# Kernel tuning notes

Measured on AMD Instinct MI355X. Metric: run time of the kernel, lower is better.

The kernel has to match this reference:

```python
import jax, jax.numpy as jnp
import numpy as np

B, T, H = 16, 512, 384   # batch, phoneme length, hidden
F, K = 384, 3            # filter size, kernel size
DMAX = 8                 # max per-token duration
L = T * DMAX             # static max expanded length (original uses real_len.max())


def conv1d_same(x, w, b):
    # x: [B, T, Cin], w: [Cout, Cin, K] (torch OIW layout), padding = K//2 both sides
    y = jax.lax.conv_general_dilated(
        x.transpose(0, 2, 1), w, window_strides=(1,),
        padding=[(K // 2, K // 2)], dimension_numbers=('NCW', 'OIW', 'NCW'))
    return y.transpose(0, 2, 1) + b


def layer_norm(x, g, b, eps=1e-5):
    mu = jnp.mean(x, axis=-1, keepdims=True)
    var = jnp.mean(jnp.square(x - mu), axis=-1, keepdims=True)
    return (x - mu) * jax.lax.rsqrt(var + eps) * g + b


def setup_inputs() -> dict:
    key = jax.random.key(0)
    ks = jax.random.split(key, 10)
    x = jax.random.normal(ks[0], (B, T, H), dtype=jnp.float32)
    # log-durations whose exp().round() gives integers in [1, DMAX]
    dur = jax.random.randint(ks[1], (B, T), 1, DMAX + 1)
    true_durations = jnp.log(dur.astype(jnp.float32))
    s1 = 1.0 / np.sqrt(H * K)
    s2 = 1.0 / np.sqrt(F * K)
    s3 = 1.0 / np.sqrt(F)
    return {
        'x': x,
        'true_durations': true_durations,
        'conv1_w': jax.random.uniform(ks[2], (F, H, K), jnp.float32, -s1, s1),
        'conv1_b': jnp.zeros((F,), jnp.float32),
        'ln1_g': jnp.ones((F,), jnp.float32),
        'ln1_b': jnp.zeros((F,), jnp.float32),
        'conv2_w': jax.random.uniform(ks[3], (F, F, K), jnp.float32, -s2, s2),
        'conv2_b': jnp.zeros((F,), jnp.float32),
        'ln2_g': jnp.ones((F,), jnp.float32),
        'ln2_b': jnp.zeros((F,), jnp.float32),
        'lin_w': jax.random.uniform(ks[4], (F, 1), jnp.float32, -s3, s3),
        'lin_b': jnp.zeros((1,), jnp.float32),
    }


def reference(x, true_durations, conv1_w, conv1_b, ln1_g, ln1_b,
              conv2_w, conv2_b, ln2_g, ln2_b, lin_w, lin_b):
    # duration predictor net (dropout in eval mode = identity)
    h = conv1d_same(x, conv1_w, conv1_b)
    h = jax.nn.gelu(layer_norm(h, ln1_g, ln1_b), approximate=False)
    h = conv1d_same(h, conv2_w, conv2_b)
    h = jax.nn.gelu(layer_norm(h, ln2_g, ln2_b), approximate=False)
    length = jax.nn.relu(h @ lin_w + lin_b)[..., 0]  # [B, T]

    # length regulation with ground-truth durations (detached ints in original)
    dur = jnp.round(jnp.exp(true_durations)).astype(jnp.int32)  # [B, T]
    ends = jnp.cumsum(dur, axis=1)          # [B, T]
    starts = ends - dur                     # [B, T]
    k = jnp.arange(L)                       # [L]
    # binary alignment: A[b,t,l] = 1 iff starts[b,t] <= l < ends[b,t]
    A = ((k >= starts[..., None]) & (k < ends[..., None])).astype(x.dtype)  # [B,T,L]
    out = jnp.einsum('bth,btl->blh', x, A)  # = (x^T @ A)^T, [B, L, H]
    return out, length
```

## Files before the change

kernel.cpp:

```cpp
#include <hip/hip_runtime.h>
#include <stdint.h>

typedef unsigned short u16;
typedef unsigned int   u32;

#define B_    16
#define T_    512
#define H_    384
#define F_    384
#define DMAX_ 8
#define L_    4096
#define KD    1152
#define M_    8192

typedef __bf16 bf16x8 __attribute__((ext_vector_type(8)));
typedef float  f32x4  __attribute__((ext_vector_type(4)));

typedef __attribute__((address_space(1))) u32 gu32;
typedef __attribute__((address_space(3))) u32 lu32;

__device__ __forceinline__ void dma16(const void* g, void* l) {
    __builtin_amdgcn_global_load_lds((gu32*)(uintptr_t)g, (lu32*)(u32)(uintptr_t)l, 16, 0, 0);
}

__device__ __forceinline__ u16 f2b(float f) {
    union { float f; u32 i; } v; v.f = f;
    u32 x = v.i;
    return (u16)((x + 0x7fffu + ((x >> 16) & 1u)) >> 16);
}

__global__ void k_prep(const float* __restrict__ td, const float* __restrict__ w1,
                       const float* __restrict__ w2, const float* __restrict__ x,
                       int* __restrict__ tmap, u16* __restrict__ Wp1,
                       u16* __restrict__ Wp2, u16* __restrict__ xb,
                       u16* __restrict__ zp) {
    int blk = blockIdx.x, tid = threadIdx.x;
    if (blk < 16) {
        __shared__ int s[T_];
        int b = blk, t = tid;
        int d = (int)roundf(expf(td[b * T_ + t]));
        if (d < 0) d = 0; if (d > DMAX_) d = DMAX_;
        int v = d;
        s[t] = v;
        __syncthreads();
        for (int off = 1; off < T_; off <<= 1) {
            int add = (t >= off) ? s[t - off] : 0;
            __syncthreads();
            v += add;
            s[t] = v;
            __syncthreads();
        }
        int end = v, start = end - d;
        for (int i = start; i < end; ++i) tmap[b * L_ + i] = t;
        int total = s[T_ - 1];
        for (int l = total + t; l < L_; l += T_) tmap[b * L_ + l] = -1;
    } else if (blk == 16) {
        zp[tid] = 0;
    } else if (blk < 17 + 1728) {
        int j = (blk - 17) * 512 + tid;
        const int n = F_ * H_ * 3;
        const float* src = (j < n) ? w1 : w2;
        u16* dst         = (j < n) ? Wp1 : Wp2;
        int jj = (j < n) ? j : j - n;
        int f = jj / (H_ * 3);
        int rem = jj % (H_ * 3);
        int c = rem / 3, kk = rem % 3;
        dst[f * KD + kk * H_ + c] = f2b(src[jj]);
    } else {
        int v = (blk - 1745) * 512 + tid;
        float4 f = *(const float4*)(x + (size_t)v * 4);
        u16 o[4] = { f2b(f.x), f2b(f.y), f2b(f.z), f2b(f.w) };
        *(uint2*)(xb + (size_t)v * 4) = *(uint2*)o;
    }
}

#define CHT 3584
#define DBO 28672

__device__ __forceinline__ void gemm_core64(u16* smem, const u16* __restrict__ src,
                                            const u16* __restrict__ Wp,
                                            const u16* __restrict__ zp,
                                            int m0, int tid, f32x4 acc[2][6]) {
    int w = tid >> 6, lane = tid & 63;
    int quad = lane >> 4, l16 = lane & 15;
    int wm = w & 1, wn = w >> 1;

    int rowA = tid >> 3;
    int qlA  = (tid & 7) ^ (rowA & 7);
    int arow = m0 + rowA;
    int bB = arow >> 9, tt = arow & 511;
    const u16* abase[3];
    #pragma unroll
    for (int kk = 0; kk < 3; ++kk) {
        int ts = tt + kk - 1;
        abase[kk] = (ts >= 0 && ts < T_) ? (src + (size_t)((bB << 9) + ts) * H_ + qlA * 8)
                                         : (zp + qlA * 8);
    }
    int adst = tid * 8;
    const u16* bbase[6];
    int bdst[6];
    #pragma unroll
    for (int p = 0; p < 6; ++p) {
        int idx = p * 512 + tid;
        int rowB = idx >> 3;
        int qlB  = (tid & 7) ^ (rowB & 7);
        bbase[p] = Wp + (size_t)rowB * KD + qlB * 8;
        bdst[p]  = (512 + idx) * 8;
    }

    int aoff[2][2], boff[6][2];
    #pragma unroll
    for (int i = 0; i < 2; ++i)
        #pragma unroll
        for (int kv = 0; kv < 2; ++kv) {
            int row = wm * 32 + i * 16 + l16;
            aoff[i][kv] = ((row << 3) | ((kv * 4 + quad) ^ (row & 7))) * 8;
        }
    #pragma unroll
    for (int j = 0; j < 6; ++j)
        #pragma unroll
        for (int kv = 0; kv < 2; ++kv) {
            int row = wn * 96 + j * 16 + l16;
            boff[j][kv] = (512 + ((row << 3) | ((kv * 4 + quad) ^ (row & 7)))) * 8;
        }

    #pragma unroll
    for (int i = 0; i < 2; ++i)
        #pragma unroll
        for (int j = 0; j < 6; ++j)
            acc[i][j] = f32x4{0.f, 0.f, 0.f, 0.f};

    {
        u16* base = smem;
        #pragma unroll
        for (int p = 0; p < 6; ++p) dma16(bbase[p], base + bdst[p]);
        dma16(abase[0], base + adst);
    }

    int kk1 = 0, s61 = 0;
    for (int s = 0; s < 18; ++s) {
        __syncthreads();
        if (s < 17) {
            if (++s61 == 6) { s61 = 0; ++kk1; }
            int koff = (s + 1) * 64;
            u16* base = smem + (((s + 1) & 1) ? DBO : 0);
            #pragma unroll
            for (int p = 0; p < 6; ++p) dma16(bbase[p] + koff, base + bdst[p]);
            dma16(abase[kk1] + s61 * 64, base + adst);
        }
        const u16* rb = smem + ((s & 1) ? DBO : 0);
        #pragma unroll
        for (int kv = 0; kv < 2; ++kv) {
            bf16x8 af0 = *(const bf16x8*)(rb + aoff[0][kv]);
            bf16x8 af1 = *(const bf16x8*)(rb + aoff[1][kv]);
            #pragma unroll
            for (int j = 0; j < 6; ++j) {
                bf16x8 bf = *(const bf16x8*)(rb + boff[j][kv]);
                acc[0][j] = __builtin_amdgcn_mfma_f32_16x16x32_bf16(af0, bf, acc[0][j], 0, 0, 0);
                acc[1][j] = __builtin_amdgcn_mfma_f32_16x16x32_bf16(af1, bf, acc[1][j], 0, 0, 0);
            }
        }
    }
    __syncthreads();
}

__launch_bounds__(512)
__global__ void k_main1(const u16* __restrict__ xb, const u16* __restrict__ Wp,
                        const float* __restrict__ bias, const float* __restrict__ g,
                        const float* __restrict__ beta, u16* __restrict__ G,
                        const u16* __restrict__ zp, const float* __restrict__ x,
                        const int* __restrict__ tmap, float* __restrict__ out0) {
    __shared__ u16 smem[2 * DBO];
    int tid = threadIdx.x;
    if (blockIdx.x >= 128) {
        int bi = blockIdx.x - 128;
        int v0 = bi * 4096;
        #pragma unroll
        for (int it = 0; it < 8; ++it) {
            int v = v0 + it * 512 + tid;
            int row = v / 96, c4 = v % 96;
            int b = row >> 12;
            int t = tmap[row];
            uint4 val = make_uint4(0u, 0u, 0u, 0u);
            if (t >= 0) val = *(const uint4*)(x + (size_t)((b << 9) + t) * H_ + c4 * 4);
            *(uint4*)(out0 + (size_t)row * H_ + c4 * 4) = val;
        }
        return;
    }
    int w = tid >> 6, lane = tid & 63;
    int quad = lane >> 4, l16 = lane & 15;
    int wm = w & 1, wn = w >> 1;
    int m0 = blockIdx.x * 64;

    f32x4 acc[2][6];
    gemm_core64(smem, xb, Wp, zp, m0, tid, acc);

    float bcol[6], gcol[6], becol[6];
    #pragma unroll
    for (int j = 0; j < 6; ++j) {
        int col = wn * 96 + j * 16 + l16;
        bcol[j] = bias[col]; gcol[j] = g[col]; becol[j] = beta[col];
    }
    float* sb  = (float*)smem;
    float* s2b = (float*)smem + 256;
    #pragma unroll
    for (int i = 0; i < 2; ++i)
        #pragma unroll
        for (int r = 0; r < 4; ++r) {
            float s = 0.f, s2 = 0.f;
            #pragma unroll
            for (int j = 0; j < 6; ++j) {
                float y = acc[i][j][r] + bcol[j];
                s += y; s2 += y * y;
            }
            #pragma unroll
            for (int off = 8; off; off >>= 1) { s += __shfl_down(s, off); s2 += __shfl_down(s2, off); }
            if (l16 == 0) {
                int rl = i * 16 + quad * 4 + r;
                sb[(wm * 4 + wn) * 32 + rl] = s; s2b[(wm * 4 + wn) * 32 + rl] = s2;
            }
        }
    __syncthreads();
    #pragma unroll
    for (int i = 0; i < 2; ++i)
        #pragma unroll
        for (int r = 0; r < 4; ++r) {
            int rl = i * 16 + quad * 4 + r;
            float S = 0.f, S2 = 0.f;
            #pragma unroll
            for (int p = 0; p < 4; ++p) { S += sb[(wm * 4 + p) * 32 + rl]; S2 += s2b[(wm * 4 + p) * 32 + rl]; }
            float mean = S * (1.f / F_);
            float var  = S2 * (1.f / F_) - mean * mean;
            float rstd = rsqrtf(var + 1e-5f);
            #pragma unroll
            for (int j = 0; j < 6; ++j) {
                int col = wn * 96 + j * 16 + l16;
                float y  = (acc[i][j][r] + bcol[j] - mean) * rstd * gcol[j] + becol[j];
                float gl = 0.5f * y * (1.f + erff(y * 0.70710678118654752f));
                G[(size_t)(m0 + wm * 32 + rl) * F_ + col] = f2b(gl);
            }
        }
}

__launch_bounds__(512)
__global__ void k_gemm2(const u16* __restrict__ G, const u16* __restrict__ Wp,
                        const float* __restrict__ bias, const float* __restrict__ g,
                        const float* __restrict__ beta, const float* __restrict__ lw,
                        const float* __restrict__ lb, float* __restrict__ out1,
                        const u16* __restrict__ zp) {
    __shared__ u16 smem[2 * DBO];
    int tid = threadIdx.x;
    int w = tid >> 6, lane = tid & 63;
    int quad = lane >> 4, l16 = lane & 15;
    int wm = w & 1, wn = w >> 1;
    int m0 = blockIdx.x * 64;

    f32x4 acc[2][6];
    gemm_core64(smem, G, Wp, zp, m0, tid, acc);

    float bcol[6], gcol[6], becol[6], lwcol[6];
    #pragma unroll
    for (int j = 0; j < 6; ++j) {
        int col = wn * 96 + j * 16 + l16;
        bcol[j] = bias[col]; gcol[j] = g[col]; becol[j] = beta[col]; lwcol[j] = lw[col];
    }
    float* sb  = (float*)smem;
    float* s2b = (float*)smem + 256;
    float* db  = (float*)smem + 512;
    #pragma unroll
    for (int i = 0; i < 2; ++i)
        #pragma unroll
        for (int r = 0; r < 4; ++r) {
            float s = 0.f, s2 = 0.f;
            #pragma unroll
            for (int j = 0; j < 6; ++j) {
                float y = acc[i][j][r] + bcol[j];
                s += y; s2 += y * y;
            }
            #pragma unroll
            for (int off = 8; off; off >>= 1) { s += __shfl_down(s, off); s2 += __shfl_down(s2, off); }
            if (l16 == 0) {
                int rl = i * 16 + quad * 4 + r;
                sb[(wm * 4 + wn) * 32 + rl] = s; s2b[(wm * 4 + wn) * 32 + rl] = s2;
            }
        }
    __syncthreads();
    #pragma unroll
    for (int i = 0; i < 2; ++i)
        #pragma unroll
        for (int r = 0; r < 4; ++r) {
            int rl = i * 16 + quad * 4 + r;
            float S = 0.f, S2 = 0.f;
            #pragma unroll
            for (int p = 0; p < 4; ++p) { S += sb[(wm * 4 + p) * 32 + rl]; S2 += s2b[(wm * 4 + p) * 32 + rl]; }
            float mean = S * (1.f / F_);
            float var  = S2 * (1.f / F_) - mean * mean;
            float rstd = rsqrtf(var + 1e-5f);
            float dot = 0.f;
            #pragma unroll
            for (int j = 0; j < 6; ++j) {
                float y  = (acc[i][j][r] + bcol[j] - mean) * rstd * gcol[j] + becol[j];
                float gl = 0.5f * y * (1.f + erff(y * 0.70710678118654752f));
                dot += gl * lwcol[j];
            }
            #pragma unroll
            for (int off = 8; off; off >>= 1) dot += __shfl_down(dot, off);
            if (l16 == 0) db[(wm * 4 + wn) * 32 + rl] = dot;
        }
    __syncthreads();
    if (tid < 64) {
        int wmv = tid >> 5, rl = tid & 31;
        float d = lb[0];
        #pragma unroll
        for (int p = 0; p < 4; ++p) d += db[(wmv * 4 + p) * 32 + rl];
        out1[m0 + tid] = fmaxf(d, 0.f);
    }
}

extern "C" void kernel_launch(void* const* d_in, const int* in_sizes, int n_in,
                              void* d_out, int out_size, void* d_ws, size_t ws_size,
                              hipStream_t stream) {
    const float* x   = (const float*)d_in[0];
    const float* td  = (const float*)d_in[1];
    const float* w1  = (const float*)d_in[2];
    const float* b1  = (const float*)d_in[3];
    const float* g1  = (const float*)d_in[4];
    const float* be1 = (const float*)d_in[5];
    const float* w2  = (const float*)d_in[6];
    const float* b2  = (const float*)d_in[7];
    const float* g2  = (const float*)d_in[8];
    const float* be2 = (const float*)d_in[9];
    const float* lw  = (const float*)d_in[10];
    const float* lb  = (const float*)d_in[11];

    float* out0 = (float*)d_out;
    float* out1 = out0 + (size_t)B_ * L_ * H_;

    char* ws = (char*)d_ws;
    size_t off = 0;
    auto carve = [&](size_t bytes) -> void* {
        void* p = ws + off;
        off = (off + bytes + 255) & ~(size_t)255;
        return p;
    };
    int*  tmap = (int*)carve((size_t)B_ * L_ * sizeof(int));
    u16*  Wp1  = (u16*)carve((size_t)F_ * KD * sizeof(u16));
    u16*  Wp2  = (u16*)carve((size_t)F_ * KD * sizeof(u16));
    u16*  xb   = (u16*)carve((size_t)M_ * H_ * sizeof(u16));
    u16*  G    = (u16*)carve((size_t)M_ * F_ * sizeof(u16));
    u16*  zp   = (u16*)carve(1024);

    k_prep<<<3281, 512, 0, stream>>>(td, w1, w2, x, tmap, Wp1, Wp2, xb, zp);
    k_main1<<<128 + 1536, 512, 0, stream>>>(xb, Wp1, b1, g1, be1, G, zp, x, tmap, out0);
    k_gemm2<<<128, 512, 0, stream>>>(G, Wp2, b2, g2, be2, lw, lb, out1, zp);
}
```

Measured before the change: 186.2 us.

## Fuse x bf16 conversion into conv1 loads and split gather across kernels

Removes the separate x→bf16 staging buffer: conv1 now loads fp32 x directly, converts to bf16 in registers and stores to LDS after the MFMA step, replacing DMA for the A tile. Weight repacking is rewritten so writes are coalesced. The length-regulation gather is split in half between the two GEMM kernels so the copy overlaps with the small 128-block gemm2 grid. Boundary rows now read fp32 from the zero pad with offsets that can exceed its 1024-byte size.

New measurement: 193.4 us. 3.9% more time.

```diff
diff --git a/kernel.cpp b/kernel.cpp
--- a/kernel.cpp
+++ b/kernel.cpp
@@ -29,10 +29,16 @@
     return (u16)((x + 0x7fffu + ((x >> 16) & 1u)) >> 16);
 }
 
+__device__ __forceinline__ bf16x8 cvt8(float4 a, float4 b) {
+    bf16x8 r;
+    r[0] = (__bf16)a.x; r[1] = (__bf16)a.y; r[2] = (__bf16)a.z; r[3] = (__bf16)a.w;
+    r[4] = (__bf16)b.x; r[5] = (__bf16)b.y; r[6] = (__bf16)b.z; r[7] = (__bf16)b.w;
+    return r;
+}
+
 __global__ void k_prep(const float* __restrict__ td, const float* __restrict__ w1,
-                       const float* __restrict__ w2, const float* __restrict__ x,
-                       int* __restrict__ tmap, u16* __restrict__ Wp1,
-                       u16* __restrict__ Wp2, u16* __restrict__ xb,
+                       const float* __restrict__ w2, int* __restrict__ tmap,
+                       u16* __restrict__ Wp1, u16* __restrict__ Wp2,
                        u16* __restrict__ zp) {
     int blk = blockIdx.x, tid = threadIdx.x;
     if (blk < 16) {
@@ -56,120 +62,28 @@
         for (int l = total + t; l < L_; l += T_) tmap[b * L_ + l] = -1;
     } else if (blk == 16) {
         zp[tid] = 0;
-    } else if (blk < 17 + 1728) {
-        int j = (blk - 17) * 512 + tid;
-        const int n = F_ * H_ * 3;
-        const float* src = (j < n) ? w1 : w2;
-        u16* dst         = (j < n) ? Wp1 : Wp2;
-        int jj = (j < n) ? j : j - n;
-        int f = jj / (H_ * 3);
-        int rem = jj % (H_ * 3);
-        int c = rem / 3, kk = rem % 3;
-        dst[f * KD + kk * H_ + c] = f2b(src[jj]);
     } else {
-        int v = (blk - 1745) * 512 + tid;
-        float4 f = *(const float4*)(x + (size_t)v * 4);
-        u16 o[4] = { f2b(f.x), f2b(f.y), f2b(f.z), f2b(f.w) };
-        *(uint2*)(xb + (size_t)v * 4) = *(uint2*)o;
+        int i = (blk - 17) * 512 + tid;
+        const int n = F_ * KD;
+        const float* src = (i < n) ? w1 : w2;
+        u16* dst         = (i < n) ? Wp1 : Wp2;
+        int ii = (i < n) ? i : i - n;
+        int f = ii / KD;
+        int rem = ii % KD;
+        int kk = rem / H_, c = rem % H_;
+        dst[ii] = f2b(src[f * KD + c * 3 + kk]);
     }
 }
 
 #define CHT 3584
 #define DBO 28672
 
-__device__ __forceinline__ void gemm_core64(u16* smem, const u16* __restrict__ src,
-                                            const u16* __restrict__ Wp,
-                                            const u16* __restrict__ zp,
-                                            int m0, int tid, f32x4 acc[2][6]) {
-    int w = tid >> 6, lane = tid & 63;
-    int quad = lane >> 4, l16 = lane & 15;
-    int wm = w & 1, wn = w >> 1;
-
-    int rowA = tid >> 3;
-    int qlA  = (tid & 7) ^ (rowA & 7);
-    int arow = m0 + rowA;
-    int bB = arow >> 9, tt = arow & 511;
-    const u16* abase[3];
-    #pragma unroll
-    for (int kk = 0; kk < 3; ++kk) {
-        int ts = tt + kk - 1;
-        abase[kk] = (ts >= 0 && ts < T_) ? (src + (size_t)((bB << 9) + ts) * H_ + qlA * 8)
-                                         : (zp + qlA * 8);
-    }
-    int adst = tid * 8;
-    const u16* bbase[6];
-    int bdst[6];
-    #pragma unroll
-    for (int p = 0; p < 6; ++p) {
-        int idx = p * 512 + tid;
-        int rowB = idx >> 3;
-        int qlB  = (tid & 7) ^ (rowB & 7);
-        bbase[p] = Wp + (size_t)rowB * KD + qlB * 8;
-        bdst[p]  = (512 + idx) * 8;
-    }
-
-    int aoff[2][2], boff[6][2];
-    #pragma unroll
-    for (int i = 0; i < 2; ++i)
-        #pragma unroll
-        for (int kv = 0; kv < 2; ++kv) {
-            int row = wm * 32 + i * 16 + l16;
-            aoff[i][kv] = ((row << 3) | ((kv * 4 + quad) ^ (row & 7))) * 8;
-        }
-    #pragma unroll
-    for (int j = 0; j < 6; ++j)
-        #pragma unroll
-        for (int kv = 0; kv < 2; ++kv) {
-            int row = wn * 96 + j * 16 + l16;
-            boff[j][kv] = (512 + ((row << 3) | ((kv * 4 + quad) ^ (row & 7)))) * 8;
-        }
-
-    #pragma unroll
-    for (int i = 0; i < 2; ++i)
-        #pragma unroll
-        for (int j = 0; j < 6; ++j)
-            acc[i][j] = f32x4{0.f, 0.f, 0.f, 0.f};
-
-    {
-        u16* base = smem;
-        #pragma unroll
-        for (int p = 0; p < 6; ++p) dma16(bbase[p], base + bdst[p]);
-        dma16(abase[0], base + adst);
-    }
-
-    int kk1 = 0, s61 = 0;
-    for (int s = 0; s < 18; ++s) {
-        __syncthreads();
-        if (s < 17) {
-            if (++s61 == 6) { s61 = 0; ++kk1; }
-            int koff = (s + 1) * 64;
-            u16* base = smem + (((s + 1) & 1) ? DBO : 0);
-            #pragma unroll
-            for (int p = 0; p < 6; ++p) dma16(bbase[p] + koff, base + bdst[p]);
-            dma16(abase[kk1] + s61 * 64, base + adst);
-        }
-        const u16* rb = smem + ((s & 1) ? DBO : 0);
-        #pragma unroll
-        for (int kv = 0; kv < 2; ++kv) {
-            bf16x8 af0 = *(const bf16x8*)(rb + aoff[0][kv]);
-            bf16x8 af1 = *(const bf16x8*)(rb + aoff[1][kv]);
-            #pragma unroll
-            for (int j = 0; j < 6; ++j) {
-                bf16x8 bf = *(const bf16x8*)(rb + boff[j][kv]);
-                acc[0][j] = __builtin_amdgcn_mfma_f32_16x16x32_bf16(af0, bf, acc[0][j], 0, 0, 0);
-                acc[1][j] = __builtin_amdgcn_mfma_f32_16x16x32_bf16(af1, bf, acc[1][j], 0, 0, 0);
-            }
-        }
-    }
-    __syncthreads();
-}
-
 __launch_bounds__(512)
-__global__ void k_main1(const u16* __restrict__ xb, const u16* __restrict__ Wp,
+__global__ void k_main1(const float* __restrict__ x, const u16* __restrict__ Wp,
                         const float* __restrict__ bias, const float* __restrict__ g,
                         const float* __restrict__ beta, u16* __restrict__ G,
-                        const u16* __restrict__ zp, const float* __restrict__ x,
-                        const int* __restrict__ tmap, float* __restrict__ out0) {
+                        const u16* __restrict__ zp, const int* __restrict__ tmap,
+                        float* __restrict__ out0) {
     __shared__ u16 smem[2 * DBO];
     int tid = threadIdx.x;
     if (blockIdx.x >= 128) {
@@ -192,8 +106,89 @@
     int wm = w & 1, wn = w >> 1;
     int m0 = blockIdx.x * 64;
 
+    int rowA = tid >> 3;
+    int qlA  = (tid & 7) ^ (rowA & 7);
+    int arow = m0 + rowA;
+    int bB = arow >> 9, tt = arow & 511;
+    const float* zpf = (const float*)zp;
+    const float* abase[3];
+    #pragma unroll
+    for (int kk = 0; kk < 3; ++kk) {
+        int ts = tt + kk - 1;
+        abase[kk] = (ts >= 0 && ts < T_) ? (x + (size_t)((bB << 9) + ts) * H_ + qlA * 8) : zpf;
+    }
+    int adst = tid * 8;
+
+    const u16* bbase[6];
+    int bdst[6];
+    #pragma unroll
+    for (int p = 0; p < 6; ++p) {
+        int idx = p * 512 + tid;
+        int rowB = idx >> 3;
+        int qlB  = (tid & 7) ^ (rowB & 7);
+        bbase[p] = Wp + (size_t)rowB * KD + qlB * 8;
+        bdst[p]  = (512 + idx) * 8;
+    }
+
+    int aoff[2][2], boff[6][2];
+    #pragma unroll
+    for (int i = 0; i < 2; ++i)
+        #pragma unroll
+        for (int kv = 0; kv < 2; ++kv) {
+            int row = wm * 32 + i * 16 + l16;
+            aoff[i][kv] = ((row << 3) | ((kv * 4 + quad) ^ (row & 7))) * 8;
+        }
+    #pragma unroll
+    for (int j = 0; j < 6; ++j)
+        #pragma unroll
+        for (int kv = 0; kv < 2; ++kv) {
+            int row = wn * 96 + j * 16 + l16;
+            boff[j][kv] = (512 + ((row << 3) | ((kv * 4 + quad) ^ (row & 7)))) * 8;
+        }
+
     f32x4 acc[2][6];
-    gemm_core64(smem, xb, Wp, zp, m0, tid, acc);
+    #pragma unroll
+    for (int i = 0; i < 2; ++i)
+        #pragma unroll
+        for (int j = 0; j < 6; ++j)
+            acc[i][j] = f32x4{0.f, 0.f, 0.f, 0.f};
+
+    {
+        float4 a0 = *(const float4*)(abase[0]);
+        float4 a1 = *(const float4*)(abase[0] + 4);
+        #pragma unroll
+        for (int p = 0; p < 6; ++p) dma16(bbase[p], smem + bdst[p]);
+        *(bf16x8*)(smem + adst) = cvt8(a0, a1);
+    }
+
+    int kk1 = 0, s61 = 0;
+    for (int s = 0; s < 18; ++s) {
+        __syncthreads();
+        float4 n0, n1;
+        u16* nbase = smem + (((s + 1) & 1) ? DBO : 0);
+        if (s < 17) {
+            if (++s61 == 6) { s61 = 0; ++kk1; }
+            int koff = (s + 1) * 64;
+            n0 = *(const float4*)(abase[kk1] + s61 * 64);
+            n1 = *(const float4*)(abase[kk1] + s61 * 64 + 4);
+            #pragma unroll
+            for (int p = 0; p < 6; ++p) dma16(bbase[p] + koff, nbase + bdst[p]);
+        }
+        const u16* rb = smem + ((s & 1) ? DBO : 0);
+        #pragma unroll
+        for (int kv = 0; kv < 2; ++kv) {
+            bf16x8 af0 = *(const bf16x8*)(rb + aoff[0][kv]);
+            bf16x8 af1 = *(const bf16x8*)(rb + aoff[1][kv]);
+            #pragma unroll
+            for (int j = 0; j < 6; ++j) {
+                bf16x8 bf = *(const bf16x8*)(rb + boff[j][kv]);
+                acc[0][j] = __builtin_amdgcn_mfma_f32_16x16x32_bf16(af0, bf, acc[0][j], 0, 0, 0);
+                acc[1][j] = __builtin_amdgcn_mfma_f32_16x16x32_bf16(af1, bf, acc[1][j], 0, 0, 0);
+            }
+        }
+        if (s < 17) *(bf16x8*)(nbase + adst) = cvt8(n0, n1);
+    }
+    __syncthreads();
 
     float bcol[6], gcol[6], becol[6];
     #pragma unroll
@@ -247,16 +242,107 @@
                         const float* __restrict__ bias, const float* __restrict__ g,
                         const float* __restrict__ beta, const float* __restrict__ lw,
                         const float* __restrict__ lb, float* __restrict__ out1,
-                        const u16* __restrict__ zp) {
+                        const u16* __restrict__ zp, const float* __restrict__ x,
+                        const int* __restrict__ tmap, float* __restrict__ out0) {
     __shared__ u16 smem[2 * DBO];
     int tid = threadIdx.x;
+    if (blockIdx.x >= 128) {
+        int bi = blockIdx.x - 128;
+        int v0 = 3145728 + bi * 4096;
+        #pragma unroll
+        for (int it = 0; it < 8; ++it) {
+            int v = v0 + it * 512 + tid;
+            int row = v / 96, c4 = v % 96;
+            int b = row >> 12;
+            int t = tmap[row];
+            uint4 val = make_uint4(0u, 0u, 0u, 0u);
+            if (t >= 0) val = *(const uint4*)(x + (size_t)((b << 9) + t) * H_ + c4 * 4);
+            *(uint4*)(out0 + (size_t)row * H_ + c4 * 4) = val;
+        }
+        return;
+    }
     int w = tid >> 6, lane = tid & 63;
     int quad = lane >> 4, l16 = lane & 15;
     int wm = w & 1, wn = w >> 1;
     int m0 = blockIdx.x * 64;
 
+    int rowA = tid >> 3;
+    int qlA  = (tid & 7) ^ (rowA & 7);
+    int arow = m0 + rowA;
+    int bB = arow >> 9, tt = arow & 511;
+    const u16* abase[3];
+    #pragma unroll
+    for (int kk = 0; kk < 3; ++kk) {
+        int ts = tt + kk - 1;
+        abase[kk] = (ts >= 0 && ts < T_) ? (G + (size_t)((bB << 9) + ts) * H_ + qlA * 8)
+                                         : (zp + qlA * 8);
+    }
+    int adst = tid * 8;
+    const u16* bbase[6];
+    int bdst[6];
+    #pragma unroll
+    for (int p = 0; p < 6; ++p) {
+        int idx = p * 512 + tid;
+        int rowB = idx >> 3;
+        int qlB  = (tid & 7) ^ (rowB & 7);
+        bbase[p] = Wp + (size_t)rowB * KD + qlB * 8;
+        bdst[p]  = (512 + idx) * 8;
+    }
+
+    int aoff[2][2], boff[6][2];
+    #pragma unroll
+    for (int i = 0; i < 2; ++i)
+        #pragma unroll
+        for (int kv = 0; kv < 2; ++kv) {
+            int row = wm * 32 + i * 16 + l16;
+            aoff[i][kv] = ((row << 3) | ((kv * 4 + quad) ^ (row & 7))) * 8;
+        }
+    #pragma unroll
+    for (int j = 0; j < 6; ++j)
+        #pragma unroll
+        for (int kv = 0; kv < 2; ++kv) {
+            int row = wn * 96 + j * 16 + l16;
+            boff[j][kv] = (512 + ((row << 3) | ((kv * 4 + quad) ^ (row & 7)))) * 8;
+        }
+
     f32x4 acc[2][6];
-    gemm_core64(smem, G, Wp, zp, m0, tid, acc);
+    #pragma unroll
+    for (int i = 0; i < 2; ++i)
+        #pragma unroll
+        for (int j = 0; j < 6; ++j)
+            acc[i][j] = f32x4{0.f, 0.f, 0.f, 0.f};
+
+    {
+        u16* base = smem;
+        #pragma unroll
+        for (int p = 0; p < 6; ++p) dma16(bbase[p], base + bdst[p]);
+        dma16(abase[0], base + adst);
+    }
+    int kk1 = 0, s61 = 0;
+    for (int s = 0; s < 18; ++s) {
+        __syncthreads();
+        if (s < 17) {
+            if (++s61 == 6) { s61 = 0; ++kk1; }
+            int koff = (s + 1) * 64;
+            u16* base = smem + (((s + 1) & 1) ? DBO : 0);
+            #pragma unroll
+            for (int p = 0; p < 6; ++p) dma16(bbase[p] + koff, base + bdst[p]);
+            dma16(abase[kk1] + s61 * 64, base + adst);
+        }
+        const u16* rb = smem + ((s & 1) ? DBO : 0);
+        #pragma unroll
+        for (int kv = 0; kv < 2; ++kv) {
+            bf16x8 af0 = *(const bf16x8*)(rb + aoff[0][kv]);
+            bf16x8 af1 = *(const bf16x8*)(rb + aoff[1][kv]);
+            #pragma unroll
+            for (int j = 0; j < 6; ++j) {
+                bf16x8 bf = *(const bf16x8*)(rb + boff[j][kv]);
+                acc[0][j] = __builtin_amdgcn_mfma_f32_16x16x32_bf16(af0, bf, acc[0][j], 0, 0, 0);
+                acc[1][j] = __builtin_amdgcn_mfma_f32_16x16x32_bf16(af1, bf, acc[1][j], 0, 0, 0);
+            }
+        }
+    }
+    __syncthreads();
 
     float bcol[6], gcol[6], becol[6], lwcol[6];
     #pragma unroll
@@ -346,11 +432,10 @@
     int*  tmap = (int*)carve((size_t)B_ * L_ * sizeof(int));
     u16*  Wp1  = (u16*)carve((size_t)F_ * KD * sizeof(u16));
     u16*  Wp2  = (u16*)carve((size_t)F_ * KD * sizeof(u16));
-    u16*  xb   = (u16*)carve((size_t)M_ * H_ * sizeof(u16));
     u16*  G    = (u16*)carve((size_t)M_ * F_ * sizeof(u16));
     u16*  zp   = (u16*)carve(1024);
 
-    k_prep<<<3281, 512, 0, stream>>>(td, w1, w2, x, tmap, Wp1, Wp2, xb, zp);
-    k_main1<<<128 + 1536, 512, 0, stream>>>(xb, Wp1, b1, g1, be1, G, zp, x, tmap, out0);
-    k_gemm2<<<128, 512, 0, stream>>>(G, Wp2, b2, g2, be2, lw, lb, out1, zp);
-}
+    k_prep<<<1745, 512, 0, stream>>>(td, w1, w2, tmap, Wp1, Wp2, zp);
+    k_main1<<<128 + 768, 512, 0, stream>>>(x, Wp1, b1, g1, be1, G, zp, tmap, out0);
+    k_gemm2<<<128 + 768, 512, 0, stream>>>(G, Wp2, b2, g2, be2, lw, lb, out1, zp, x, tmap, out0);
+}
```
